# Kernel tuning notes

Hardware: AMD Instinct MI355X
Metric: run time of the kernel (lower is better)

Reference implementation:

```python
import jax, jax.numpy as jnp
import numpy as np

# Uniform batch of B graphs, N nodes each, C features, skip-window size FS
B, N, C, FS = 64, 512, 128, 16
RES = N - 1            # number of window rows per graph (unfold1d with stride 1)
TAU_A, TAU_B, TOT_EPOCHS = 10.0, 0.1, 100.0
EPS = 1e-20
NEG = -1e9


def setup_inputs() -> dict:
    key = jax.random.key(0)
    k1, k2, k3, k4 = jax.random.split(key, 4)
    x = jax.random.normal(k1, (B * N, C), dtype=jnp.float32)
    edge_index = jax.random.randint(k2, (2, 524288), 0, B * N, dtype=jnp.int32)
    score_w = jax.random.normal(k3, (C, 1), dtype=jnp.float32)       # TopKPool Linear weight
    att_params = jax.random.normal(k4, (2 * C, 1), dtype=jnp.float32)  # SKipPool att_params
    return {"x": x, "edge_index": edge_index, "score_w": score_w,
            "att_params": att_params, "epoch": 10}


def _forward(x, score_w, att_params, epoch):
    tau0 = TAU_A * (TAU_B / TAU_A) ** (epoch / TOT_EPOCHS)

    # ---- TopKPool scorer (init_ratio -> 1.0: keep all nodes, rank-sort per graph) ----
    scores = (x @ score_w)[:, 0] / jnp.linalg.norm(score_w)   # [B*N]
    sv = scores.reshape(B, N)
    order = jnp.argsort(-sv, axis=1)                           # descending perm per graph
    xg = jnp.take_along_axis(x.reshape(B, N, C), order[:, :, None], axis=1)  # [B,N,C]
    scores_ranked = jnp.tanh(jnp.take_along_axis(sv, order, axis=1))         # [B,N]

    # ---- skip-window edge construction (unfold1d semantics): row r -> dests r..r+FS-1 ----
    r = jnp.arange(RES)
    j = jnp.arange(FS)
    dest = r[:, None] + j[None, :]            # [RES,FS]
    valid = dest < N                          # padded positions masked (inf/zero rows)
    destc = jnp.minimum(dest, N - 1)

    xs = xg[:, :RES, None, :]                                  # [B,RES,1,C] sources
    xd = jnp.where(valid[None, :, :, None], xg[:, destc], 0.0)  # [B,RES,FS,C] dests

    # getDM_ei: RBF kernel over edge distances (sigma=1); masked edges -> 0 (inf row)
    d = jnp.linalg.norm(xs - xd, axis=-1)                      # [B,RES,FS]
    kmat = jnp.where(valid[None], jnp.exp(-d / 2.0), 0.0) - EPS

    # getSM_ei: attention score via att_params on [x_src || x_dst]
    a_src, a_dst = att_params[:C, 0], att_params[C:, 0]
    atts = (xg[:, :RES] @ a_src)[:, :, None] + jnp.einsum('brjc,c->brj', xd, a_dst)
    atts = jnp.where(valid[None], atts, NEG)
    w_att = jax.nn.softmax(atts / tau0, axis=-1)               # tau-annealed row softmax

    q = kmat * w_att                                           # combined edge score [B,RES,FS]
    qm = jnp.where(valid[None], q, NEG)
    w_row = jnp.max(qm, axis=-1)                               # best-match score per row (scatterSort top-1)
    jumps = 1 + jnp.argmax(qm[:, :, 1:], axis=-1).astype(jnp.int32)  # data-dependent stride in [1,FS-1]

    # ---- sequential pivot chaining (innerLoopStar): pivot -> pivot + jump[pivot] ----
    def chain(xg_b, w_b, sr_b, jumps_b):
        def step(carry, _):
            p, acc = carry
            active = p < RES
            pc = jnp.minimum(p, RES - 1)
            wv = jnp.where(active, w_b[pc] * sr_b[pc], 0.0)
            acc = acc + wv * xg_b[pc]
            p = jnp.where(active, p + jumps_b[pc], p)
            return (p, acc), None
        (pf, acc), _ = jax.lax.scan(step, (jnp.int32(0), jnp.zeros((C,), xg_b.dtype)),
                                    None, length=RES)
        return acc

    pooled = jax.vmap(chain)(xg, w_row, scores_ranked[:, :RES], jumps)  # [B,C]
    return pooled


def reference(x, edge_index, score_w, att_params, epoch):
    # edge_index only feeds the scorer's filter_adj in the original (structure unused here)
    return _forward(x, score_w, att_params, epoch)
```

## Files before the change

### kernel.cpp

```cpp
#include <hip/hip_runtime.h>
#include <math.h>

#define B_   64
#define N_   512
#define C_   128
#define FS_  16
#define RES_ 511
#define CHUNK_ 64
#define HALO_  15
#define MAXR_  (CHUNK_ + HALO_)
#define RSTRIDE_ 132
#define RSTRIDE16_ 136

__device__ __forceinline__ float bf2f(unsigned short u) {
  union { unsigned int i; float f; } v;
  v.i = ((unsigned int)u) << 16;
  return v.f;
}
__device__ __forceinline__ float bflo(unsigned int u) {
  union { unsigned int i; float f; } v; v.i = u << 16; return v.f;
}
__device__ __forceinline__ float bfhi(unsigned int u) {
  union { unsigned int i; float f; } v; v.i = u & 0xFFFF0000u; return v.f;
}

__device__ __forceinline__ float2 ld2(const void* p, int idx, int mode) {
  if (mode) return ((const float2*)p)[idx];
  ushort2 u = ((const ushort2*)p)[idx];
  return make_float2(bf2f(u.x), bf2f(u.y));
}
__device__ __forceinline__ float ld1(const void* p, int idx, int mode) {
  if (mode) return ((const float*)p)[idx];
  return bf2f(((const unsigned short*)p)[idx]);
}
__device__ __forceinline__ float4 ld4(const void* p, int idx4, int mode) {
  if (mode) return ((const float4*)p)[idx4];
  ushort4 u = ((const ushort4*)p)[idx4];
  return make_float4(bf2f(u.x), bf2f(u.y), bf2f(u.z), bf2f(u.w));
}

__device__ __forceinline__ double wred(double v) {
#pragma unroll
  for (int m = 32; m; m >>= 1) v += __shfl_xor(v, m, 64);
  return v;
}
__device__ __forceinline__ float wredf(float v) {
#pragma unroll
  for (int m = 32; m; m >>= 1) v += __shfl_xor(v, m, 64);
  return v;
}

#define RORF1(v) __builtin_bit_cast(float, __builtin_amdgcn_update_dpp( \
    0, __builtin_bit_cast(int, v), 0x121, 0xF, 0xF, false))
#define RORF2(v) __builtin_bit_cast(float, __builtin_amdgcn_update_dpp( \
    0, __builtin_bit_cast(int, v), 0x122, 0xF, 0xF, false))
#define RORF4(v) __builtin_bit_cast(float, __builtin_amdgcn_update_dpp( \
    0, __builtin_bit_cast(int, v), 0x124, 0xF, 0xF, false))
#define RORF8(v) __builtin_bit_cast(float, __builtin_amdgcn_update_dpp( \
    0, __builtin_bit_cast(int, v), 0x128, 0xF, 0xF, false))

__device__ __forceinline__ float rmax16(float v) {
  v = fmaxf(v, RORF1(v));
  v = fmaxf(v, RORF2(v));
  v = fmaxf(v, RORF4(v));
  v = fmaxf(v, RORF8(v));
  return v;
}
__device__ __forceinline__ float rsum16(float v) {
  v = v + RORF1(v);
  v = v + RORF2(v);
  v = v + RORF4(v);
  v = v + RORF8(v);
  return v;
}

__device__ __forceinline__ int detect_w0(const unsigned short* p, int lane) {
  int e = (p[lane] >> 7) & 0xFF;
  unsigned long long m = __ballot(e >= 100 && e <= 140);
  return (__popcll(m) >= 48) ? 0 : 1;
}

__device__ __forceinline__ float get_epoch(const int* ep) {
  int ei = ep[0];
  if (ei >= 0 && ei <= 1000000) return (float)ei;
  union { int i; float f; } u; u.i = ei;
  return (u.f >= 0.f && u.f <= 1e6f) ? u.f : 10.f;
}

__global__ __launch_bounds__(256) void k_scores(
    const void* __restrict__ x, const void* __restrict__ w,
    float* __restrict__ sc)
{
  __shared__ int s_modes[2];
  const int t = threadIdx.x, lane = t & 63;
  if (t < 64) {
    int mx_ = detect_w0((const unsigned short*)x, lane);
    int mw_ = detect_w0((const unsigned short*)w, lane);
    if (t == 0) { s_modes[0] = mx_; s_modes[1] = mw_; }
  }
  __syncthreads();
  const int mode_x = s_modes[0], mode_w = s_modes[1];
  const int wid = (blockIdx.x * blockDim.x + t) >> 6;
  const int node0 = wid * 4;

  const float2 wv2 = ld2(w, lane, mode_w);
  const double nww = wred((double)wv2.x * wv2.x + (double)wv2.y * wv2.y);
  const float nrm32 = (float)sqrt(nww);

#pragma unroll
  for (int i = 0; i < 4; ++i) {
    float2 xv = ld2(x, (node0 + i) * 64 + lane, mode_x);
    double s  = wred((double)xv.x * wv2.x + (double)xv.y * wv2.y);
    if (lane == 0) sc[node0 + i] = ((float)s) / nrm32;
  }
}

__global__ __launch_bounds__(256) void k_sort(
    const float* __restrict__ sc, int* __restrict__ order,
    float* __restrict__ srk)
{
  __shared__ __align__(16) float sl[N_];
  __shared__ int part[4][CHUNK_];
  const int blk = blockIdx.x, b = blk >> 3, ch = blk & 7;
  const int bN = b * N_, t = threadIdx.x;
  sl[t]       = sc[bN + t];
  sl[t + 256] = sc[bN + t + 256];
  __syncthreads();
  const int n = t & 63, p = t >> 6;
  const int g = ch * CHUNK_ + n;
  const float my = sl[g];
  const float4* sl4 = (const float4*)sl;
  int rank = 0;
#pragma unroll 4
  for (int k4 = p * 32; k4 < p * 32 + 32; ++k4) {
    float4 v = sl4[k4];
    int k = k4 * 4;
    rank += (int)((v.x > my) || (v.x == my && k     < g));
    rank += (int)((v.y > my) || (v.y == my && k + 1 < g));
    rank += (int)((v.z > my) || (v.z == my && k + 2 < g));
    rank += (int)((v.w > my) || (v.w == my && k + 3 < g));
  }
  part[p][n] = rank;
  __syncthreads();
  if (t < CHUNK_) {
    const int gg = ch * CHUNK_ + t;
    const int r = part[0][t] + part[1][t] + part[2][t] + part[3][t];
    order[bN + r] = gg;
    srk[bN + r]   = tanhf(sl[gg]);
  }
}

__global__ __launch_bounds__(1024, 8) void k_att(
    const void* __restrict__ x, const void* __restrict__ a,
    const int* __restrict__ order, const int* __restrict__ ep,
    float* __restrict__ wrw, int* __restrict__ jmp)
{
  __shared__ __align__(16) float rows[MAXR_ * RSTRIDE_];
  __shared__ float ads_l[MAXR_];
  __shared__ float asr_l[CHUNK_];
  __shared__ int   ord_l[MAXR_];
  __shared__ int   s_modes[2];
  __shared__ float s_invtau;

  unsigned short* rows16 = (unsigned short*)rows;

  const int blk = blockIdx.x;
  const int b = blk >> 3;
  const int cr0 = (blk & 7) * CHUNK_;
  const int bN = b * N_;
  const int t = threadIdx.x;
  const int lane = t & 63, wv = t >> 6;
  const int nrows = min(N_ - cr0, MAXR_);

  if (t < 64) {
    int mx_ = detect_w0((const unsigned short*)x, lane);
    int ma_ = detect_w0((const unsigned short*)a, lane);
    if (t == 0) {
      s_modes[0] = mx_; s_modes[1] = ma_;
      float evv = get_epoch(ep);
      s_invtau = (float)(1.0 / (10.0 * pow(0.01, (double)evv / 100.0)));
    }
  }
  if (t < nrows) {
    int o = order[bN + cr0 + t];
    ord_l[t] = min(max(o, 0), N_ - 1);
  }
  __syncthreads();
  const int mode_x = s_modes[0], mode_a = s_modes[1];
  const float inv_tau = s_invtau;

  if (mode_x == 0) {
    const int rl0 = t >> 4, c8 = t & 15;
    for (int rl = rl0; rl < nrows; rl += 64) {
      uint4 v = ((const uint4*)x)[(bN + ord_l[rl]) * 16 + c8];
      *(uint4*)&rows16[rl * RSTRIDE16_ + c8 * 8] = v;
    }
  } else {
    const int rl0 = t >> 5, c4 = t & 31;
    for (int rl = rl0; rl < nrows; rl += 32) {
      float4 v = ld4(x, (bN + ord_l[rl]) * 32 + c4, 1);
      float* dst = &rows[rl * RSTRIDE_ + c4 * 4];
      dst[0] = v.x; dst[1] = v.y; dst[2] = v.z; dst[3] = v.w;
    }
  }
  __syncthreads();

  {
    const float2 sv2 = ld2(a, lane, mode_a);
    const float2 dv2 = ld2(a, 64 + lane, mode_a);
    for (int rl = wv; rl < nrows; rl += 16) {
      float2 xr;
      if (mode_x == 0) {
        ushort2 u = *(const ushort2*)&rows16[rl * RSTRIDE16_ + 2 * lane];
        xr = make_float2(bf2f(u.x), bf2f(u.y));
      } else {
        xr = *(const float2*)&rows[rl * RSTRIDE_ + 2 * lane];
      }
      float da = wredf(xr.x * sv2.x + xr.y * sv2.y);
      float dd = wredf(xr.x * dv2.x + xr.y * dv2.y);
      if (lane == 0) {
        ads_l[rl] = dd;
        if (rl < CHUNK_) asr_l[rl] = da;
      }
    }
  }
  __syncthreads();

  const int j = lane & 15, cg4 = lane >> 4;
  const int nr = min(CHUNK_, RES_ - cr0);
  int cnt = nr - wv * 4; cnt = max(0, min(4, cnt));

#pragma unroll 2
  for (int ii = 0; ii < cnt; ++ii) {
    const int rloc = wv * 4 + ii;
    const int r = cr0 + rloc;
    const int dest = r + j;
    const bool valid = dest < N_;
    const int dl = (valid ? dest : (N_ - 1)) - cr0;

    double p0 = 0.0, p1 = 0.0, p2 = 0.0, p3 = 0.0;
    if (mode_x == 0) {
      const unsigned short* sp = &rows16[rloc * RSTRIDE16_ + cg4 * 32];
      const unsigned short* dp = &rows16[dl   * RSTRIDE16_ + cg4 * 32];
#pragma unroll
      for (int c = 0; c < 4; ++c) {
        uint4 s = *(const uint4*)(sp + c * 8);
        uint4 d = *(const uint4*)(dp + c * 8);
        float e0 = bflo(s.x) - bflo(d.x), e1 = bfhi(s.x) - bfhi(d.x);
        float e2 = bflo(s.y) - bflo(d.y), e3 = bfhi(s.y) - bfhi(d.y);
        p0 += (double)(e0 * e0); p1 += (double)(e1 * e1);
        p2 += (double)(e2 * e2); p3 += (double)(e3 * e3);
        float f0 = bflo(s.z) - bflo(d.z), f1 = bfhi(s.z) - bfhi(d.z);
        float f2 = bflo(s.w) - bflo(d.w), f3 = bfhi(s.w) - bfhi(d.w);
        p0 += (double)(f0 * f0); p1 += (double)(f1 * f1);
        p2 += (double)(f2 * f2); p3 += (double)(f3 * f3);
      }
    } else {
      const float* srcp = &rows[rloc * RSTRIDE_ + cg4 * 32];
      const float* dstp = &rows[dl   * RSTRIDE_ + cg4 * 32];
#pragma unroll
      for (int c = 0; c < 8; ++c) {
        float4 s4 = *(const float4*)(srcp + c * 4);
        float4 d4 = *(const float4*)(dstp + c * 4);
        float e0 = s4.x - d4.x, e1 = s4.y - d4.y;
        float e2 = s4.z - d4.z, e3 = s4.w - d4.w;
        float q0 = e0 * e0, q1 = e1 * e1, q2 = e2 * e2, q3 = e3 * e3;
        p0 += (double)q0; p1 += (double)q1; p2 += (double)q2; p3 += (double)q3;
      }
    }
    double dacc = (p0 + p1) + (p2 + p3);
    dacc += __shfl_xor(dacc, 16, 64);
    dacc += __shfl_xor(dacc, 32, 64);

    float d32 = sqrtf((float)dacc);
    float kkj = valid ? (__expf(-0.5f * d32) - 1e-20f) : -1e-20f;
    float aaj = valid ? (asr_l[rloc] + ads_l[dl]) : -1e9f;
    float ttj = aaj * inv_tau;

    float mx = rmax16(ttj);
    float eej = __expf(ttj - mx);
    float ssum = rsum16(eej);
    ssum = __shfl(ssum, lane & 48, 64);
    float q  = kkj * (eej * (1.0f / ssum));
    float qm = valid ? q : -1e9f;

    float qe = (j == 0) ? -INFINITY : qm;
    float m1 = rmax16(qe);
    float q0v = __shfl(qm, lane & 48, 64);
    float wr = fmaxf(m1, q0v);
    unsigned long long mask = __ballot(qe == m1);
    int bj = __builtin_ctz((unsigned)(mask & 0xFFFEu));

    if (lane == 0) {
      wrw[bN + r] = wr;
      jmp[bN + r] = bj;
    }
  }
}

__global__ __launch_bounds__(512) void k_chain(
    const void* __restrict__ x, const float* __restrict__ wrw,
    const float* __restrict__ srk, const int* __restrict__ jmp,
    const int* __restrict__ order, float* __restrict__ out)
{
  __shared__ int   tab[9][N_];
  __shared__ int   ol[N_];
  __shared__ float wl[N_];
  __shared__ float sl2[N_];
  __shared__ float cl[N_];
  __shared__ int   rl[N_];
  __shared__ int   Pcnt;
  __shared__ int   s_mode;

  const int b = blockIdx.x, t = threadIdx.x;
  if (t < 64) {
    int mx_ = detect_w0((const unsigned short*)x, t);
    if (t == 0) s_mode = mx_;
  }

  ol[t] = min(max(order[b * N_ + t], 0), N_ - 1);
  if (t < RES_) {
    wl[t]  = wrw[b * N_ + t];
    sl2[t] = srk[b * N_ + t];
    int jv = jmp[b * N_ + t];
    jv = min(max(jv, 1), FS_ - 1);
    tab[0][t] = min(t + jv, RES_);
  } else {
    tab[0][t] = RES_;
  }
  if (t == 0) Pcnt = RES_;
  __syncthreads();
  const int mode_x = s_mode;
#pragma unroll
  for (int k = 1; k < 9; ++k) {
    int v = tab[k - 1][tab[k - 1][t]];
    tab[k][t] = v;
    __syncthreads();
  }
  int node = 0;
#pragma unroll
  for (int k = 0; k < 9; ++k)
    if ((t >> k) & 1) node = tab[k][node];
  bool valid = (node < RES_);
  cl[t] = valid ? wl[node] * sl2[node] : 0.0f;
  rl[t] = valid ? ol[node] : 0;
  if (!valid) atomicMin(&Pcnt, t);
  __syncthreads();

  if (t < C_) {
    const int P = Pcnt;
    float acc = 0.f;
    int i = 0;
    for (; i + 8 <= P; i += 8) {
      float c0 = cl[i],     c1 = cl[i + 1], c2 = cl[i + 2], c3 = cl[i + 3];
      float c4 = cl[i + 4], c5 = cl[i + 5], c6 = cl[i + 6], c7 = cl[i + 7];
      int   r0 = rl[i],     r1 = rl[i + 1], r2 = rl[i + 2], r3 = rl[i + 3];
      int   r4 = rl[i + 4], r5 = rl[i + 5], r6 = rl[i + 6], r7 = rl[i + 7];
      float x0 = ld1(x, (b * N_ + r0) * C_ + t, mode_x);
      float x1 = ld1(x, (b * N_ + r1) * C_ + t, mode_x);
      float x2 = ld1(x, (b * N_ + r2) * C_ + t, mode_x);
      float x3 = ld1(x, (b * N_ + r3) * C_ + t, mode_x);
      float x4 = ld1(x, (b * N_ + r4) * C_ + t, mode_x);
      float x5 = ld1(x, (b * N_ + r5) * C_ + t, mode_x);
      float x6 = ld1(x, (b * N_ + r6) * C_ + t, mode_x);
      float x7 = ld1(x, (b * N_ + r7) * C_ + t, mode_x);
      acc = acc + c0 * x0;
      acc = acc + c1 * x1;
      acc = acc + c2 * x2;
      acc = acc + c3 * x3;
      acc = acc + c4 * x4;
      acc = acc + c5 * x5;
      acc = acc + c6 * x6;
      acc = acc + c7 * x7;
    }
    for (; i + 4 <= P; i += 4) {
      float c0 = cl[i],     c1 = cl[i + 1], c2 = cl[i + 2], c3 = cl[i + 3];
      int   r0 = rl[i],     r1 = rl[i + 1], r2 = rl[i + 2], r3 = rl[i + 3];
      float x0 = ld1(x, (b * N_ + r0) * C_ + t, mode_x);
      float x1 = ld1(x, (b * N_ + r1) * C_ + t, mode_x);
      float x2 = ld1(x, (b * N_ + r2) * C_ + t, mode_x);
      float x3 = ld1(x, (b * N_ + r3) * C_ + t, mode_x);
      acc = acc + c0 * x0;
      acc = acc + c1 * x1;
      acc = acc + c2 * x2;
      acc = acc + c3 * x3;
    }
    for (; i < P; ++i)
      acc = acc + cl[i] * ld1(x, (b * N_ + rl[i]) * C_ + t, mode_x);
    out[b * C_ + t] = acc;
  }
}

extern "C" void kernel_launch(void* const* d_in, const int* in_sizes, int n_in,
                              void* d_out, int out_size, void* d_ws, size_t ws_size,
                              hipStream_t stream) {
  const void* x = nullptr; const void* w = nullptr; const void* a = nullptr;
  const int* ep = nullptr;
  for (int i = 0; i < n_in; ++i) {
    int s = in_sizes[i];
    if      (s == B_ * N_ * C_) x  = d_in[i];
    else if (s == C_)           w  = d_in[i];
    else if (s == 2 * C_)       a  = d_in[i];
    else if (s == 1)            ep = (const int*)d_in[i];
  }
  if (!x)  x  = d_in[0];
  if (!w)  w  = d_in[2];
  if (!a)  a  = d_in[3];
  if (!ep) ep = (const int*)d_in[4];
  (void)out_size; (void)ws_size;

  float* ws = (float*)d_ws;
  const int NN = B_ * N_;
  float* sc    = ws;
  int*   order = (int*)(ws + NN);
  float* srk   = ws + 2 * NN;
  float* wrw   = ws + 3 * NN;
  int*   jmp   = (int*)(ws + 4 * NN);

  k_scores<<<B_ * N_ / 16, 256, 0, stream>>>(x, w, sc);
  k_sort<<<B_ * 8, 256, 0, stream>>>(sc, order, srk);
  k_att<<<B_ * 8, 1024, 0, stream>>>(x, a, order, ep, wrw, jmp);
  k_chain<<<B_, N_, 0, stream>>>(x, wrw, srk, jmp, order, (float*)d_out);
}
```

Before: 119.1 us.

## Compute pairwise distances via norm expansion with bf16 dot2 and float accumulation

Rewrites the squared distance ||s-d||^2 as ||s||^2 + ||d||^2 - 2 s·d. The per-row norms are precomputed in the existing attention-projection pass, and the cross term uses the v_dot2_f32_bf16 instruction on packed bf16 pairs. It also replaces double-precision accumulation with float FMA in both the bf16 and fp32 paths, which removes slow FP64 work and conversions. The expansion risks catastrophic cancellation when s and d are close; this is partly handled by forcing j==0 to zero and clamping to non-negative, and it adds a small shared array of norms.

Measured after the change: 113.6 us. 4.6% less time.

```diff
diff --git a/kernel.cpp b/kernel.cpp
--- a/kernel.cpp
+++ b/kernel.cpp
@@ -85,6 +85,17 @@
   if (ei >= 0 && ei <= 1000000) return (float)ei;
   union { int i; float f; } u; u.i = ei;
   return (u.f >= 0.f && u.f <= 1e6f) ? u.f : 10.f;
+}
+
+#define USE_DOT2_ASM 1
+__device__ __forceinline__ float dot2bf(float acc, unsigned int s,
+                                        unsigned int d) {
+#if USE_DOT2_ASM
+  asm("v_dot2_f32_bf16 %0, %1, %2, %0" : "+v"(acc) : "v"(s), "v"(d));
+  return acc;
+#else
+  return fmaf(bfhi(s), bfhi(d), fmaf(bflo(s), bflo(d), acc));
+#endif
 }
 
 __global__ __launch_bounds__(256) void k_scores(
@@ -158,6 +169,7 @@
   __shared__ __align__(16) float rows[MAXR_ * RSTRIDE_];
   __shared__ float ads_l[MAXR_];
   __shared__ float asr_l[CHUNK_];
+  __shared__ float nrm_l[MAXR_];
   __shared__ int   ord_l[MAXR_];
   __shared__ int   s_modes[2];
   __shared__ float s_invtau;
@@ -209,17 +221,20 @@
     const float2 sv2 = ld2(a, lane, mode_a);
     const float2 dv2 = ld2(a, 64 + lane, mode_a);
     for (int rl = wv; rl < nrows; rl += 16) {
-      float2 xr;
+      float xlo, xhi;
       if (mode_x == 0) {
-        ushort2 u = *(const ushort2*)&rows16[rl * RSTRIDE16_ + 2 * lane];
-        xr = make_float2(bf2f(u.x), bf2f(u.y));
+        unsigned int u = *(const unsigned int*)&rows16[rl * RSTRIDE16_ + 2 * lane];
+        xlo = bflo(u); xhi = bfhi(u);
       } else {
-        xr = *(const float2*)&rows[rl * RSTRIDE_ + 2 * lane];
+        float2 xr = *(const float2*)&rows[rl * RSTRIDE_ + 2 * lane];
+        xlo = xr.x; xhi = xr.y;
       }
-      float da = wredf(xr.x * sv2.x + xr.y * sv2.y);
-      float dd = wredf(xr.x * dv2.x + xr.y * dv2.y);
+      float da = wredf(xlo * sv2.x + xhi * sv2.y);
+      float dd = wredf(xlo * dv2.x + xhi * dv2.y);
+      float nn = wredf(fmaf(xlo, xlo, xhi * xhi));
       if (lane == 0) {
         ads_l[rl] = dd;
+        nrm_l[rl] = nn;
         if (rl < CHUNK_) asr_l[rl] = da;
       }
     }
@@ -238,41 +253,44 @@
     const bool valid = dest < N_;
     const int dl = (valid ? dest : (N_ - 1)) - cr0;
 
-    double p0 = 0.0, p1 = 0.0, p2 = 0.0, p3 = 0.0;
+    float dacc;
     if (mode_x == 0) {
       const unsigned short* sp = &rows16[rloc * RSTRIDE16_ + cg4 * 32];
       const unsigned short* dp = &rows16[dl   * RSTRIDE16_ + cg4 * 32];
+      float g0 = 0.f, g1 = 0.f;
 #pragma unroll
       for (int c = 0; c < 4; ++c) {
-        uint4 s = *(const uint4*)(sp + c * 8);
-        uint4 d = *(const uint4*)(dp + c * 8);
-        float e0 = bflo(s.x) - bflo(d.x), e1 = bfhi(s.x) - bfhi(d.x);
-        float e2 = bflo(s.y) - bflo(d.y), e3 = bfhi(s.y) - bfhi(d.y);
-        p0 += (double)(e0 * e0); p1 += (double)(e1 * e1);
-        p2 += (double)(e2 * e2); p3 += (double)(e3 * e3);
-        float f0 = bflo(s.z) - bflo(d.z), f1 = bfhi(s.z) - bfhi(d.z);
-        float f2 = bflo(s.w) - bflo(d.w), f3 = bfhi(s.w) - bfhi(d.w);
-        p0 += (double)(f0 * f0); p1 += (double)(f1 * f1);
-        p2 += (double)(f2 * f2); p3 += (double)(f3 * f3);
+        uint4 s = ((const uint4*)sp)[c];
+        uint4 d = ((const uint4*)dp)[c];
+        g0 = dot2bf(g0, s.x, d.x);
+        g1 = dot2bf(g1, s.y, d.y);
+        g0 = dot2bf(g0, s.z, d.z);
+        g1 = dot2bf(g1, s.w, d.w);
       }
+      float gg = g0 + g1;
+      gg += __shfl_xor(gg, 16, 64);
+      gg += __shfl_xor(gg, 32, 64);
+      dacc = nrm_l[rloc] + nrm_l[dl] - 2.f * gg;
     } else {
       const float* srcp = &rows[rloc * RSTRIDE_ + cg4 * 32];
       const float* dstp = &rows[dl   * RSTRIDE_ + cg4 * 32];
+      float q0 = 0.f, q1 = 0.f, q2 = 0.f, q3 = 0.f;
 #pragma unroll
       for (int c = 0; c < 8; ++c) {
         float4 s4 = *(const float4*)(srcp + c * 4);
         float4 d4 = *(const float4*)(dstp + c * 4);
         float e0 = s4.x - d4.x, e1 = s4.y - d4.y;
         float e2 = s4.z - d4.z, e3 = s4.w - d4.w;
-        float q0 = e0 * e0, q1 = e1 * e1, q2 = e2 * e2, q3 = e3 * e3;
-        p0 += (double)q0; p1 += (double)q1; p2 += (double)q2; p3 += (double)q3;
+        q0 = fmaf(e0, e0, q0); q1 = fmaf(e1, e1, q1);
+        q2 = fmaf(e2, e2, q2); q3 = fmaf(e3, e3, q3);
       }
-    }
-    double dacc = (p0 + p1) + (p2 + p3);
-    dacc += __shfl_xor(dacc, 16, 64);
-    dacc += __shfl_xor(dacc, 32, 64);
-
-    float d32 = sqrtf((float)dacc);
+      float qq = (q0 + q1) + (q2 + q3);
+      qq += __shfl_xor(qq, 16, 64);
+      qq += __shfl_xor(qq, 32, 64);
+      dacc = qq;
+    }
+
+    float d32 = (j == 0) ? 0.f : sqrtf(fmaxf(dacc, 0.f));
     float kkj = valid ? (__expf(-0.5f * d32) - 1e-20f) : -1e-20f;
     float aaj = valid ? (asr_l[rloc] + ads_l[dl]) : -1e9f;
     float ttj = aaj * inv_tau;
```
